# Optimization experiments

Hardware: AMD Instinct MI355X
Metric: run time of the kernel (lower is better)

## Reference

```python
import jax, jax.numpy as jnp
import numpy as np

HIDDEN = 1024
HEADS = 16
HEAD_DIM = HIDDEN // HEADS


def setup_inputs() -> dict:
    key = jax.random.key(0)
    ks = jax.random.split(key, 9)
    B, S = 2, 2048
    std = 1.0 / np.sqrt(HIDDEN)
    inp = {
        'hidden_states': jax.random.normal(ks[0], (B, S, HIDDEN), dtype=jnp.float32),
        'attention_mask': jnp.ones((B, S), dtype=jnp.int32),
        'wq': jax.random.normal(ks[1], (HIDDEN, HIDDEN), dtype=jnp.float32) * std,
        'bq': jnp.zeros((HIDDEN,), dtype=jnp.float32),
        'wk': jax.random.normal(ks[2], (HIDDEN, HIDDEN), dtype=jnp.float32) * std,
        'bk': jnp.zeros((HIDDEN,), dtype=jnp.float32),
        'wv': jax.random.normal(ks[3], (HIDDEN, HIDDEN), dtype=jnp.float32) * std,
        'bv': jnp.zeros((HIDDEN,), dtype=jnp.float32),
        'wo': jax.random.normal(ks[4], (HIDDEN, HIDDEN), dtype=jnp.float32) * std,
        'bo': jnp.zeros((HIDDEN,), dtype=jnp.float32),
    }
    return inp


def reference(hidden_states, attention_mask, wq, bq, wk, bk, wv, bv, wo, bo):
    B, S, H = hidden_states.shape
    def heads(x):  # [B,S,H] -> [B,nh,S,hd]
        return x.reshape(B, S, HEADS, HEAD_DIM).transpose(0, 2, 1, 3)
    q = heads(hidden_states @ wq + bq)
    k = heads(hidden_states @ wk + bk)
    v = heads(hidden_states @ wv + bv)
    scores = jnp.einsum('bhqd,bhkd->bhqk', q, k) / np.sqrt(HEAD_DIM).astype(np.float32)
    causal = jnp.tril(jnp.ones((S, S), dtype=bool))  # True = keep
    keep = causal[None, None] & (attention_mask[:, None, None, :] != 0)
    scores = jnp.where(keep, scores, -jnp.inf)
    probs = jax.nn.softmax(scores, axis=-1)
    out = jnp.einsum('bhqk,bhkd->bhqd', probs, v)  # [B,nh,S,hd]
    out = out.transpose(0, 2, 1, 3).reshape(B, S, H)
    return out @ wo + bo
```

## Files before the change

kernel.cpp:

```cpp
#include <hip/hip_runtime.h>

#define HID   1024
#define SLEN  2048
#define NHEAD 16
#define HDIM  64
#define SC2L  0.18033688f

typedef unsigned short u16;
typedef _Float16 f16;
using bf16x8 = __attribute__((ext_vector_type(8))) short;
using f16x4  = __attribute__((ext_vector_type(4))) f16;
using f16x8  = __attribute__((ext_vector_type(8))) f16;
using f32x4  = __attribute__((ext_vector_type(4))) float;

typedef __attribute__((address_space(1))) void gvoid;
typedef __attribute__((address_space(3))) void lvoid;

__device__ __forceinline__ u16 f2bf(float f) {
  union { float f; unsigned u; } v; v.f = f;
  unsigned u = v.u;
  return (u16)((u + 0x7fffu + ((u >> 16) & 1u)) >> 16);
}
__device__ __forceinline__ float bf2f(u16 b) {
  union { unsigned u; float f; } v; v.u = ((unsigned)b) << 16;
  return v.f;
}

__device__ __forceinline__ void async_ld16(const u16* g, u16* l) {
  __builtin_amdgcn_global_load_lds((gvoid*)g, (lvoid*)l, 16, 0, 0);
}

__global__ __launch_bounds__(256) void prep_kernel(const float* __restrict__ x,
                                                   const float* __restrict__ wq,
                                                   const float* __restrict__ wk,
                                                   const float* __restrict__ wv,
                                                   const float* __restrict__ wo,
                                                   u16* __restrict__ xb,
                                                   u16* __restrict__ wt) {
  const int tid = threadIdx.x;
  if (blockIdx.z == 4) {
    const int bid = blockIdx.y * 32 + blockIdx.x;
#pragma unroll
    for (int it = 0; it < 4; ++it) {
      const int i = bid * 1024 + it * 256 + tid;
      float4 v = ((const float4*)x)[i];
      ushort4 o;
      o.x = f2bf(v.x); o.y = f2bf(v.y); o.z = f2bf(v.z); o.w = f2bf(v.w);
      ((ushort4*)xb)[i] = o;
    }
    return;
  }
  const float* src = (blockIdx.z == 0) ? wq : (blockIdx.z == 1) ? wk
                   : (blockIdx.z == 2) ? wv : wo;
  u16* dst = wt + (size_t)blockIdx.z * (HID * HID);
  __shared__ float tile[32][33];
  const int n0 = blockIdx.x * 32, k0 = blockIdx.y * 32;
  const int xx = tid & 31, yy = tid >> 5;
  for (int i = yy; i < 32; i += 8)
    tile[i][xx] = src[(size_t)(k0 + i) * HID + n0 + xx];
  __syncthreads();
  for (int i = yy; i < 32; i += 8)
    dst[(size_t)(n0 + i) * HID + k0 + xx] = f2bf(tile[xx][i]);
}

__global__ __launch_bounds__(256) void gemm_qkv_kernel(const u16* __restrict__ A,
                                                       const u16* __restrict__ Bt,
                                                       const float* __restrict__ bq,
                                                       const float* __restrict__ bk,
                                                       const float* __restrict__ bv,
                                                       u16* __restrict__ Qb,
                                                       u16* __restrict__ Kb,
                                                       u16* __restrict__ Vb) {
  __shared__ u16 sA[128 * 32];
  __shared__ u16 sB[128 * 32];
  const int tid  = threadIdx.x;
  const int wave = tid >> 6, lane = tid & 63;
  const int quad = lane >> 4, l16 = lane & 15;
  const int n0g = blockIdx.x * 128;
  const int region = blockIdx.x >> 3;
  const int colbase = (blockIdx.x & 7) * 128;
  const int m0 = blockIdx.y * 128;
  const int wm = (wave & 1) * 64, wn = (wave >> 1) * 64;

  f32x4 acc[4][4] = {};
  const int srow = lane >> 2;
  const int scol = (lane & 3) * 8;

  for (int kt = 0; kt < HID; kt += 32) {
    __syncthreads();
    for (int c = wave; c < 8; c += 4) {
      async_ld16(A  + (size_t)(m0  + c * 16 + srow) * HID + kt + scol, &sA[c * 512]);
      async_ld16(Bt + (size_t)(n0g + c * 16 + srow) * HID + kt + scol, &sB[c * 512]);
    }
    __syncthreads();

    bf16x8 af[4], bfr[4];
#pragma unroll
    for (int t = 0; t < 4; ++t) {
      af[t]  = *(const bf16x8*)&sA[(wm + t * 16 + l16) * 32 + quad * 8];
      bfr[t] = *(const bf16x8*)&sB[(wn + t * 16 + l16) * 32 + quad * 8];
    }
#pragma unroll
    for (int mt = 0; mt < 4; ++mt)
#pragma unroll
      for (int nt = 0; nt < 4; ++nt)
        acc[mt][nt] = __builtin_amdgcn_mfma_f32_16x16x32_bf16(af[mt], bfr[nt],
                                                              acc[mt][nt], 0, 0, 0);
  }

  const float* bias = (region == 0) ? bq : (region == 1) ? bk : bv;
  u16* C = (region == 0) ? Qb : (region == 1) ? Kb : Vb;
  float bvv[4];
#pragma unroll
  for (int nt = 0; nt < 4; ++nt) bvv[nt] = bias[colbase + wn + nt * 16 + l16];
#pragma unroll
  for (int mt = 0; mt < 4; ++mt)
#pragma unroll
    for (int r = 0; r < 4; ++r) {
      const int row = m0 + wm + mt * 16 + quad * 4 + r;
#pragma unroll
      for (int nt = 0; nt < 4; ++nt) {
        const int col = colbase + wn + nt * 16 + l16;
        C[(size_t)row * HID + col] = f2bf(acc[mt][nt][r] + bvv[nt]);
      }
    }
}

__global__ __launch_bounds__(256) void gemm_o_kernel(const u16* __restrict__ A,
                                                     const u16* __restrict__ Bt,
                                                     const float* __restrict__ bias,
                                                     float* __restrict__ Cf) {
  __shared__ u16 sA[64 * 32];
  __shared__ u16 sB[128 * 32];
  const int tid  = threadIdx.x;
  const int wave = tid >> 6, lane = tid & 63;
  const int quad = lane >> 4, l16 = lane & 15;
  const int n0 = blockIdx.x * 128;
  const int m0 = blockIdx.y * 64;
  const int wn = wave * 32;

  f32x4 acc[4][2] = {};
  const int srow = lane >> 2;
  const int scol = (lane & 3) * 8;

  for (int kt = 0; kt < HID; kt += 32) {
    __syncthreads();
    for (int c = wave; c < 12; c += 4) {
      if (c < 4) async_ld16(A  + (size_t)(m0 + c * 16 + srow) * HID + kt + scol, &sA[c * 512]);
      else       async_ld16(Bt + (size_t)(n0 + (c - 4) * 16 + srow) * HID + kt + scol,
                            &sB[(c - 4) * 512]);
    }
    __syncthreads();

    bf16x8 af[4], bfr[2];
#pragma unroll
    for (int t = 0; t < 4; ++t)
      af[t] = *(const bf16x8*)&sA[(t * 16 + l16) * 32 + quad * 8];
#pragma unroll
    for (int t = 0; t < 2; ++t)
      bfr[t] = *(const bf16x8*)&sB[(wn + t * 16 + l16) * 32 + quad * 8];
#pragma unroll
    for (int mt = 0; mt < 4; ++mt)
#pragma unroll
      for (int nt = 0; nt < 2; ++nt)
        acc[mt][nt] = __builtin_amdgcn_mfma_f32_16x16x32_bf16(af[mt], bfr[nt],
                                                              acc[mt][nt], 0, 0, 0);
  }

  float bvv[2];
#pragma unroll
  for (int nt = 0; nt < 2; ++nt) bvv[nt] = bias[n0 + wn + nt * 16 + l16];
#pragma unroll
  for (int mt = 0; mt < 4; ++mt)
#pragma unroll
    for (int r = 0; r < 4; ++r) {
      const int row = m0 + mt * 16 + quad * 4 + r;
#pragma unroll
      for (int nt = 0; nt < 2; ++nt)
        Cf[(size_t)row * HID + n0 + wn + nt * 16 + l16] = acc[mt][nt][r] + bvv[nt];
    }
}

__global__ __launch_bounds__(256) void transpose_v_kernel(const u16* __restrict__ V,
                                                          u16* __restrict__ Vt) {
  const int s0 = blockIdx.x * 64, h = blockIdx.y, b = blockIdx.z;
  __shared__ u16 sh[64 * 72];
  const int tid = threadIdx.x;
#pragma unroll
  for (int i = 0; i < 2; ++i) {
    const int id = tid + i * 256;
    const int row = id >> 3, c = id & 7;
    *(bf16x8*)&sh[row * 72 + c * 8] =
        *(const bf16x8*)(V + (size_t)(b * SLEN + s0 + row) * HID + h * HDIM + c * 8);
  }
  __syncthreads();
#pragma unroll
  for (int i = 0; i < 2; ++i) {
    const int id = tid + i * 256;
    const int d = id >> 3, c = id & 7;
    ushort4 out2[2];
    u16* op = (u16*)out2;
#pragma unroll
    for (int e = 0; e < 8; ++e) {
      const int p = c * 8 + e;
      const int nt = (p >> 2) & 3, qd = p >> 4, jj = p & 3;
      const int s_local = nt * 16 + qd * 4 + jj;
      f16 hv = (f16)bf2f(sh[s_local * 72 + d]);
      union { f16 h; u16 u; } cv; cv.h = hv;
      op[e] = cv.u;
    }
    *(bf16x8*)(Vt + (size_t)((b * NHEAD + h) * HDIM + d) * SLEN + s0 + c * 8) =
        *(bf16x8*)out2;
  }
}

__global__ __launch_bounds__(256, 4) void flash_attn_kernel(const u16* __restrict__ Q,
                                                            const u16* __restrict__ K,
                                                            const u16* __restrict__ Vt,
                                                            const int* __restrict__ mask,
                                                            u16* __restrict__ O) {
  const int h = blockIdx.y, b = blockIdx.z;
  const int qt = (blockIdx.x + 2 * h + b) & 31;
  const int tid  = threadIdx.x;
  const int wave = tid >> 6, lane = tid & 63;
  const int quad = lane >> 4, l16 = lane & 15;
  const int mrow = wave * 16;
  const int q0 = qt * 64;

  __shared__ u16 Ks[2][64 * 72];
  __shared__ u16 Vts[2][64 * 72];
  __shared__ float maskadd[2][64];

  const int prow = tid >> 3;
  const int pcol = (tid & 7) * 8;

  const u16* Kh  = K  + (size_t)b * SLEN * HID + h * HDIM;
  const u16* Vth = Vt + (size_t)((b * NHEAD + h) * HDIM) * SLEN;

  const u16* qbase = Q + (size_t)(b * SLEN + q0 + mrow + l16) * HID + h * HDIM + quad * 8;
  const bf16x8 qa0 = *(const bf16x8*)qbase;
  const bf16x8 qa1 = *(const bf16x8*)(qbase + 32);

  f32x4 oacc[4] = {};
  float l_run = 0.f;

  bf16x8 kr0, kr1, vr0, vr1;
  int mreg = 0;
  {
    kr0 = *(const bf16x8*)(Kh + (size_t)prow * HID + pcol);
    kr1 = *(const bf16x8*)(Kh + (size_t)(prow + 32) * HID + pcol);
    vr0 = *(const bf16x8*)(Vth + (size_t)prow * SLEN + pcol);
    vr1 = *(const bf16x8*)(Vth + (size_t)(prow + 32) * SLEN + pcol);
    if (tid < 64) mreg = mask[b * SLEN + tid];
  }

  for (int j = 0; j <= qt; ++j) {
    const int buf = j & 1;
    *(bf16x8*)&Ks[buf][prow * 72 + pcol]         = kr0;
    *(bf16x8*)&Ks[buf][(prow + 32) * 72 + pcol]  = kr1;
    *(bf16x8*)&Vts[buf][prow * 72 + pcol]        = vr0;
    *(bf16x8*)&Vts[buf][(prow + 32) * 72 + pcol] = vr1;
    if (tid < 64) maskadd[buf][tid] = mreg ? 0.f : -1e30f;
    __syncthreads();

    if (j < qt) {
      kr0 = *(const bf16x8*)(Kh + (size_t)((j + 1) * 64 + prow) * HID + pcol);
      kr1 = *(const bf16x8*)(Kh + (size_t)((j + 1) * 64 + prow + 32) * HID + pcol);
      vr0 = *(const bf16x8*)(Vth + (size_t)prow * SLEN + (j + 1) * 64 + pcol);
      vr1 = *(const bf16x8*)(Vth + (size_t)(prow + 32) * SLEN + (j + 1) * 64 + pcol);
      if (tid < 64) mreg = mask[b * SLEN + (j + 1) * 64 + tid];
    }

    float p[4][4];
#pragma unroll
    for (int nt = 0; nt < 4; ++nt) {
      const bf16x8 kb0 = *(const bf16x8*)&Ks[buf][(nt * 16 + l16) * 72 + quad * 8];
      const bf16x8 kb1 = *(const bf16x8*)&Ks[buf][(nt * 16 + l16) * 72 + 32 + quad * 8];
      f32x4 z = {0.f, 0.f, 0.f, 0.f};
      z = __builtin_amdgcn_mfma_f32_16x16x32_bf16(kb0, qa0, z, 0, 0, 0);
      z = __builtin_amdgcn_mfma_f32_16x16x32_bf16(kb1, qa1, z, 0, 0, 0);
      const float4 ma = *(const float4*)&maskadd[buf][nt * 16 + quad * 4];
      const float* map = (const float*)&ma;
#pragma unroll
      for (int r = 0; r < 4; ++r)
        p[nt][r] = exp2f(fmaf(z[r], SC2L, map[r]));
    }
    if (j == qt) {
      const int qloc = mrow + l16;
#pragma unroll
      for (int nt = 0; nt < 4; ++nt)
#pragma unroll
        for (int r = 0; r < 4; ++r)
          if (nt * 16 + quad * 4 + r > qloc) p[nt][r] = 0.f;
    }

    f16x4 pb[4];
#pragma unroll
    for (int nt = 0; nt < 4; ++nt) {
      l_run += (p[nt][0] + p[nt][1]) + (p[nt][2] + p[nt][3]);
      pb[nt][0] = (f16)p[nt][0]; pb[nt][1] = (f16)p[nt][1];
      pb[nt][2] = (f16)p[nt][2]; pb[nt][3] = (f16)p[nt][3];
    }

#pragma unroll
    for (int mt = 0; mt < 4; ++mt) {
      const int vbase = (mt * 16 + l16) * 72 + quad * 16;
      const f16x8 v01 = *(const f16x8*)&Vts[buf][vbase];
      const f16x8 v23 = *(const f16x8*)&Vts[buf][vbase + 8];
      const f16x4 a0 = __builtin_shufflevector(v01, v01, 0, 1, 2, 3);
      const f16x4 a1 = __builtin_shufflevector(v01, v01, 4, 5, 6, 7);
      const f16x4 a2 = __builtin_shufflevector(v23, v23, 0, 1, 2, 3);
      const f16x4 a3 = __builtin_shufflevector(v23, v23, 4, 5, 6, 7);
      oacc[mt] = __builtin_amdgcn_mfma_f32_16x16x16f16(a0, pb[0], oacc[mt], 0, 0, 0);
      oacc[mt] = __builtin_amdgcn_mfma_f32_16x16x16f16(a1, pb[1], oacc[mt], 0, 0, 0);
      oacc[mt] = __builtin_amdgcn_mfma_f32_16x16x16f16(a2, pb[2], oacc[mt], 0, 0, 0);
      oacc[mt] = __builtin_amdgcn_mfma_f32_16x16x16f16(a3, pb[3], oacc[mt], 0, 0, 0);
    }
  }

  l_run += __shfl_xor(l_run, 16);
  l_run += __shfl_xor(l_run, 32);
  const float inv = 1.f / l_run;

  const int q = q0 + mrow + l16;
#pragma unroll
  for (int mt = 0; mt < 4; ++mt) {
    ushort4 o;
    o.x = f2bf(oacc[mt][0] * inv);
    o.y = f2bf(oacc[mt][1] * inv);
    o.z = f2bf(oacc[mt][2] * inv);
    o.w = f2bf(oacc[mt][3] * inv);
    *(ushort4*)(O + (size_t)(b * SLEN + q) * HID + h * HDIM + mt * 16 + quad * 4) = o;
  }
}

extern "C" void kernel_launch(void* const* d_in, const int* in_sizes, int n_in,
                              void* d_out, int out_size, void* d_ws, size_t ws_size,
                              hipStream_t stream) {
  const float* x    = (const float*)d_in[0];
  const int*   mask = (const int*)d_in[1];
  const float* wq   = (const float*)d_in[2];
  const float* bq   = (const float*)d_in[3];
  const float* wk   = (const float*)d_in[4];
  const float* bk   = (const float*)d_in[5];
  const float* wv   = (const float*)d_in[6];
  const float* bv   = (const float*)d_in[7];
  const float* wo   = (const float*)d_in[8];
  const float* bo   = (const float*)d_in[9];
  float* out = (float*)d_out;

  char* ws = (char*)d_ws;
  u16* XBF = (u16*)(ws);
  u16* WT  = (u16*)(ws + (8u  << 20));
  u16* QBF = (u16*)(ws + (16u << 20));
  u16* KBF = (u16*)(ws + (24u << 20));
  u16* VBF = (u16*)(ws + (32u << 20));
  u16* VTT = (u16*)(ws);
  u16* ATT = (u16*)(ws + (32u << 20));

  prep_kernel<<<dim3(32, 32, 5), 256, 0, stream>>>(x, wq, wk, wv, wo, XBF, WT);
  gemm_qkv_kernel<<<dim3(24, 32), 256, 0, stream>>>(XBF, WT, bq, bk, bv, QBF, KBF, VBF);
  transpose_v_kernel<<<dim3(32, NHEAD, 2), 256, 0, stream>>>(VBF, VTT);
  flash_attn_kernel<<<dim3(32, NHEAD, 2), 256, 0, stream>>>(QBF, KBF, VTT, mask, ATT);
  gemm_o_kernel<<<dim3(8, 64), 256, 0, stream>>>(ATT, WT + (3u << 20), bo, out);
}
```

Measured before the change: 216.2 us.

## Fuse V transpose into attention, split KV across waves, pair causal q-tiles

The separate V-transpose kernel is removed. The attention kernel now transposes V and converts it to fp16 inside shared memory while staging each tile. Each block handles two query tiles (qt and 31-qt) to balance causal work, and halves the grid. Within a tile, each wave takes a 16-key slice of the KV block for all 64 queries instead of 16 queries over all keys, so partial outputs and row sums must be combined through shared memory at the end. In exchange it carries more accumulator registers (occupancy hint lowered to 2), scattered 2-byte LDS stores, and an extra reduction with several barriers.

```diff
diff --git a/kernel.cpp b/kernel.cpp
--- a/kernel.cpp
+++ b/kernel.cpp
@@ -5,12 +5,13 @@
 #define NHEAD 16
 #define HDIM  64
 #define SC2L  0.18033688f
+#define KPAD  72
+#define VPAD  68
 
 typedef unsigned short u16;
 typedef _Float16 f16;
 using bf16x8 = __attribute__((ext_vector_type(8))) short;
 using f16x4  = __attribute__((ext_vector_type(4))) f16;
-using f16x8  = __attribute__((ext_vector_type(8))) f16;
 using f32x4  = __attribute__((ext_vector_type(4))) float;
 
 typedef __attribute__((address_space(1))) void gvoid;
@@ -21,9 +22,10 @@
   unsigned u = v.u;
   return (u16)((u + 0x7fffu + ((u >> 16) & 1u)) >> 16);
 }
-__device__ __forceinline__ float bf2f(u16 b) {
+__device__ __forceinline__ u16 bf2h(u16 b) {
   union { unsigned u; float f; } v; v.u = ((unsigned)b) << 16;
-  return v.f;
+  union { f16 h; u16 u; } c; c.h = (f16)v.f;
+  return c.u;
 }
 
 __device__ __forceinline__ void async_ld16(const u16* g, u16* l) {
@@ -181,156 +183,168 @@
     }
 }
 
-__global__ __launch_bounds__(256) void transpose_v_kernel(const u16* __restrict__ V,
-                                                          u16* __restrict__ Vt) {
-  const int s0 = blockIdx.x * 64, h = blockIdx.y, b = blockIdx.z;
-  __shared__ u16 sh[64 * 72];
-  const int tid = threadIdx.x;
-#pragma unroll
-  for (int i = 0; i < 2; ++i) {
-    const int id = tid + i * 256;
-    const int row = id >> 3, c = id & 7;
-    *(bf16x8*)&sh[row * 72 + c * 8] =
-        *(const bf16x8*)(V + (size_t)(b * SLEN + s0 + row) * HID + h * HDIM + c * 8);
-  }
-  __syncthreads();
-#pragma unroll
-  for (int i = 0; i < 2; ++i) {
-    const int id = tid + i * 256;
-    const int d = id >> 3, c = id & 7;
-    ushort4 out2[2];
-    u16* op = (u16*)out2;
-#pragma unroll
-    for (int e = 0; e < 8; ++e) {
-      const int p = c * 8 + e;
-      const int nt = (p >> 2) & 3, qd = p >> 4, jj = p & 3;
-      const int s_local = nt * 16 + qd * 4 + jj;
-      f16 hv = (f16)bf2f(sh[s_local * 72 + d]);
-      union { f16 h; u16 u; } cv; cv.h = hv;
-      op[e] = cv.u;
-    }
-    *(bf16x8*)(Vt + (size_t)((b * NHEAD + h) * HDIM + d) * SLEN + s0 + c * 8) =
-        *(bf16x8*)out2;
-  }
-}
-
-__global__ __launch_bounds__(256, 4) void flash_attn_kernel(const u16* __restrict__ Q,
+__global__ __launch_bounds__(256, 2) void flash_attn_kernel(const u16* __restrict__ Q,
                                                             const u16* __restrict__ K,
-                                                            const u16* __restrict__ Vt,
+                                                            const u16* __restrict__ V,
                                                             const int* __restrict__ mask,
                                                             u16* __restrict__ O) {
-  const int h = blockIdx.y, b = blockIdx.z;
-  const int qt = (blockIdx.x + 2 * h + b) & 31;
+  const int xb = blockIdx.x, h = blockIdx.y, b = blockIdx.z;
   const int tid  = threadIdx.x;
   const int wave = tid >> 6, lane = tid & 63;
   const int quad = lane >> 4, l16 = lane & 15;
-  const int mrow = wave * 16;
-  const int q0 = qt * 64;
-
-  __shared__ u16 Ks[2][64 * 72];
-  __shared__ u16 Vts[2][64 * 72];
+
+  __shared__ u16 Ks[2][64 * KPAD];
+  __shared__ u16 Vt[2][64 * VPAD];
   __shared__ float maskadd[2][64];
-
-  const int prow = tid >> 3;
-  const int pcol = (tid & 7) * 8;
-
-  const u16* Kh  = K  + (size_t)b * SLEN * HID + h * HDIM;
-  const u16* Vth = Vt + (size_t)((b * NHEAD + h) * HDIM) * SLEN;
-
-  const u16* qbase = Q + (size_t)(b * SLEN + q0 + mrow + l16) * HID + h * HDIM + quad * 8;
-  const bf16x8 qa0 = *(const bf16x8*)qbase;
-  const bf16x8 qa1 = *(const bf16x8*)(qbase + 32);
-
-  f32x4 oacc[4] = {};
-  float l_run = 0.f;
-
-  bf16x8 kr0, kr1, vr0, vr1;
-  int mreg = 0;
-  {
-    kr0 = *(const bf16x8*)(Kh + (size_t)prow * HID + pcol);
-    kr1 = *(const bf16x8*)(Kh + (size_t)(prow + 32) * HID + pcol);
-    vr0 = *(const bf16x8*)(Vth + (size_t)prow * SLEN + pcol);
-    vr1 = *(const bf16x8*)(Vth + (size_t)(prow + 32) * SLEN + pcol);
-    if (tid < 64) mreg = mask[b * SLEN + tid];
-  }
-
-  for (int j = 0; j <= qt; ++j) {
-    const int buf = j & 1;
-    *(bf16x8*)&Ks[buf][prow * 72 + pcol]         = kr0;
-    *(bf16x8*)&Ks[buf][(prow + 32) * 72 + pcol]  = kr1;
-    *(bf16x8*)&Vts[buf][prow * 72 + pcol]        = vr0;
-    *(bf16x8*)&Vts[buf][(prow + 32) * 72 + pcol] = vr1;
-    if (tid < 64) maskadd[buf][tid] = mreg ? 0.f : -1e30f;
-    __syncthreads();
-
-    if (j < qt) {
-      kr0 = *(const bf16x8*)(Kh + (size_t)((j + 1) * 64 + prow) * HID + pcol);
-      kr1 = *(const bf16x8*)(Kh + (size_t)((j + 1) * 64 + prow + 32) * HID + pcol);
-      vr0 = *(const bf16x8*)(Vth + (size_t)prow * SLEN + (j + 1) * 64 + pcol);
-      vr1 = *(const bf16x8*)(Vth + (size_t)(prow + 32) * SLEN + (j + 1) * 64 + pcol);
-      if (tid < 64) mreg = mask[b * SLEN + (j + 1) * 64 + tid];
-    }
-
-    float p[4][4];
+  __shared__ float lbuf[4][64];
+  float* Obuf0 = (float*)&Ks[0][0];
+  float* Obuf1 = (float*)&Vt[0][0];
+
+  const u16* Kh = K + (size_t)b * SLEN * HID + h * HDIM;
+  const u16* Vh = V + (size_t)b * SLEN * HID + h * HDIM;
+
+  const int srow = tid >> 2;
+  const int sc8  = (tid & 3) * 8;
+
+  for (int phase = 0; phase < 2; ++phase) {
+    const int qt = phase ? (31 - xb) : xb;
+    const int q0 = qt * 64;
+
+    bf16x8 qb[4][2];
 #pragma unroll
     for (int nt = 0; nt < 4; ++nt) {
-      const bf16x8 kb0 = *(const bf16x8*)&Ks[buf][(nt * 16 + l16) * 72 + quad * 8];
-      const bf16x8 kb1 = *(const bf16x8*)&Ks[buf][(nt * 16 + l16) * 72 + 32 + quad * 8];
-      f32x4 z = {0.f, 0.f, 0.f, 0.f};
-      z = __builtin_amdgcn_mfma_f32_16x16x32_bf16(kb0, qa0, z, 0, 0, 0);
-      z = __builtin_amdgcn_mfma_f32_16x16x32_bf16(kb1, qa1, z, 0, 0, 0);
-      const float4 ma = *(const float4*)&maskadd[buf][nt * 16 + quad * 4];
+      const u16* qp = Q + (size_t)(b * SLEN + q0 + nt * 16 + l16) * HID + h * HDIM + quad * 8;
+      qb[nt][0] = *(const bf16x8*)qp;
+      qb[nt][1] = *(const bf16x8*)(qp + 32);
+    }
+
+    f32x4 oacc[4][4] = {};
+    float l_part[4] = {0.f, 0.f, 0.f, 0.f};
+
+    bf16x8 kr0, kr1, vr0, vr1;
+    int mreg = 0;
+    {
+      const u16* kg = Kh + (size_t)srow * HID + sc8;
+      kr0 = *(const bf16x8*)kg;  kr1 = *(const bf16x8*)(kg + 32);
+      const u16* vg = Vh + (size_t)srow * HID + sc8;
+      vr0 = *(const bf16x8*)vg;  vr1 = *(const bf16x8*)(vg + 32);
+      if (tid < 64) mreg = mask[b * SLEN + tid];
+    }
+
+    for (int j = 0; j <= qt; ++j) {
+      const int buf = j & 1;
+      *(bf16x8*)&Ks[buf][srow * KPAD + sc8]      = kr0;
+      *(bf16x8*)&Ks[buf][srow * KPAD + sc8 + 32] = kr1;
+      {
+        const u16* v0 = (const u16*)&vr0;
+        const u16* v1 = (const u16*)&vr1;
+#pragma unroll
+        for (int e = 0; e < 8; ++e) {
+          Vt[buf][(sc8 + e) * VPAD + srow]      = bf2h(v0[e]);
+          Vt[buf][(sc8 + e + 32) * VPAD + srow] = bf2h(v1[e]);
+        }
+      }
+      if (tid < 64) maskadd[buf][tid] = mreg ? 0.f : -1e30f;
+      __syncthreads();
+
+      if (j < qt) {
+        const u16* kg = Kh + (size_t)((j + 1) * 64 + srow) * HID + sc8;
+        kr0 = *(const bf16x8*)kg;  kr1 = *(const bf16x8*)(kg + 32);
+        const u16* vg = Vh + (size_t)((j + 1) * 64 + srow) * HID + sc8;
+        vr0 = *(const bf16x8*)vg;  vr1 = *(const bf16x8*)(vg + 32);
+        if (tid < 64) mreg = mask[b * SLEN + (j + 1) * 64 + tid];
+      }
+
+      const bf16x8 ka0 = *(const bf16x8*)&Ks[buf][(wave * 16 + l16) * KPAD + quad * 8];
+      const bf16x8 ka1 = *(const bf16x8*)&Ks[buf][(wave * 16 + l16) * KPAD + quad * 8 + 32];
+      const float4 ma  = *(const float4*)&maskadd[buf][wave * 16 + quad * 4];
       const float* map = (const float*)&ma;
-#pragma unroll
-      for (int r = 0; r < 4; ++r)
-        p[nt][r] = exp2f(fmaf(z[r], SC2L, map[r]));
-    }
-    if (j == qt) {
-      const int qloc = mrow + l16;
-#pragma unroll
-      for (int nt = 0; nt < 4; ++nt)
+
+      float p[4][4];
+#pragma unroll
+      for (int nt = 0; nt < 4; ++nt) {
+        f32x4 z = {0.f, 0.f, 0.f, 0.f};
+        z = __builtin_amdgcn_mfma_f32_16x16x32_bf16(ka0, qb[nt][0], z, 0, 0, 0);
+        z = __builtin_amdgcn_mfma_f32_16x16x32_bf16(ka1, qb[nt][1], z, 0, 0, 0);
 #pragma unroll
         for (int r = 0; r < 4; ++r)
-          if (nt * 16 + quad * 4 + r > qloc) p[nt][r] = 0.f;
-    }
-
-    f16x4 pb[4];
+          p[nt][r] = exp2f(fmaf(z[r], SC2L, map[r]));
+      }
+      if (j == qt) {
+#pragma unroll
+        for (int nt = 0; nt < 4; ++nt)
+#pragma unroll
+          for (int r = 0; r < 4; ++r)
+            if (wave * 16 + quad * 4 + r > nt * 16 + l16) p[nt][r] = 0.f;
+      }
+
+      f16x4 pb[4];
+#pragma unroll
+      for (int nt = 0; nt < 4; ++nt) {
+        l_part[nt] += (p[nt][0] + p[nt][1]) + (p[nt][2] + p[nt][3]);
+        pb[nt][0] = (f16)p[nt][0]; pb[nt][1] = (f16)p[nt][1];
+        pb[nt][2] = (f16)p[nt][2]; pb[nt][3] = (f16)p[nt][3];
+      }
+
+#pragma unroll
+      for (int dt = 0; dt < 4; ++dt) {
+        const f16x4 va = *(const f16x4*)&Vt[buf][(dt * 16 + l16) * VPAD + wave * 16 + quad * 4];
+#pragma unroll
+        for (int nt = 0; nt < 4; ++nt)
+          oacc[dt][nt] = __builtin_amdgcn_mfma_f32_16x16x16f16(va, pb[nt], oacc[dt][nt], 0, 0, 0);
+      }
+    }
+
 #pragma unroll
     for (int nt = 0; nt < 4; ++nt) {
-      l_run += (p[nt][0] + p[nt][1]) + (p[nt][2] + p[nt][3]);
-      pb[nt][0] = (f16)p[nt][0]; pb[nt][1] = (f16)p[nt][1];
-      pb[nt][2] = (f16)p[nt][2]; pb[nt][3] = (f16)p[nt][3];
-    }
-
-#pragma unroll
-    for (int mt = 0; mt < 4; ++mt) {
-      const int vbase = (mt * 16 + l16) * 72 + quad * 16;
-      const f16x8 v01 = *(const f16x8*)&Vts[buf][vbase];
-      const f16x8 v23 = *(const f16x8*)&Vts[buf][vbase + 8];
-      const f16x4 a0 = __builtin_shufflevector(v01, v01, 0, 1, 2, 3);
-      const f16x4 a1 = __builtin_shufflevector(v01, v01, 4, 5, 6, 7);
-      const f16x4 a2 = __builtin_shufflevector(v23, v23, 0, 1, 2, 3);
-      const f16x4 a3 = __builtin_shufflevector(v23, v23, 4, 5, 6, 7);
-      oacc[mt] = __builtin_amdgcn_mfma_f32_16x16x16f16(a0, pb[0], oacc[mt], 0, 0, 0);
-      oacc[mt] = __builtin_amdgcn_mfma_f32_16x16x16f16(a1, pb[1], oacc[mt], 0, 0, 0);
-      oacc[mt] = __builtin_amdgcn_mfma_f32_16x16x16f16(a2, pb[2], oacc[mt], 0, 0, 0);
-      oacc[mt] = __builtin_amdgcn_mfma_f32_16x16x16f16(a3, pb[3], oacc[mt], 0, 0, 0);
-    }
-  }
-
-  l_run += __shfl_xor(l_run, 16);
-  l_run += __shfl_xor(l_run, 32);
-  const float inv = 1.f / l_run;
-
-  const int q = q0 + mrow + l16;
-#pragma unroll
-  for (int mt = 0; mt < 4; ++mt) {
-    ushort4 o;
-    o.x = f2bf(oacc[mt][0] * inv);
-    o.y = f2bf(oacc[mt][1] * inv);
-    o.z = f2bf(oacc[mt][2] * inv);
-    o.w = f2bf(oacc[mt][3] * inv);
-    *(ushort4*)(O + (size_t)(b * SLEN + q) * HID + h * HDIM + mt * 16 + quad * 4) = o;
+      l_part[nt] += __shfl_xor(l_part[nt], 16);
+      l_part[nt] += __shfl_xor(l_part[nt], 32);
+    }
+    __syncthreads();
+
+    if (quad == 0)
+#pragma unroll
+      for (int nt = 0; nt < 4; ++nt) lbuf[wave][nt * 16 + l16] = l_part[nt];
+
+    if ((wave & 1) == 0) {
+      float* ob = (wave == 0) ? Obuf0 : Obuf1;
+#pragma unroll
+      for (int dt = 0; dt < 4; ++dt)
+#pragma unroll
+        for (int nt = 0; nt < 4; ++nt)
+#pragma unroll
+          for (int r = 0; r < 4; ++r)
+            ob[(dt * 16 + quad * 4 + r) * 65 + nt * 16 + l16] = oacc[dt][nt][r];
+    }
+    __syncthreads();
+    if (wave & 1) {
+      float* ob = (wave == 1) ? Obuf0 : Obuf1;
+#pragma unroll
+      for (int dt = 0; dt < 4; ++dt)
+#pragma unroll
+        for (int nt = 0; nt < 4; ++nt)
+#pragma unroll
+          for (int r = 0; r < 4; ++r)
+            ob[(dt * 16 + quad * 4 + r) * 65 + nt * 16 + l16] += oacc[dt][nt][r];
+    }
+    __syncthreads();
+
+    {
+      const int q  = tid >> 2;
+      const int dc = tid & 3;
+      const float l = lbuf[0][q] + lbuf[1][q] + lbuf[2][q] + lbuf[3][q];
+      const float inv = 1.f / l;
+      u16 ob[16];
+#pragma unroll
+      for (int e = 0; e < 16; ++e) {
+        const int d = dc * 16 + e;
+        ob[e] = f2bf((Obuf0[d * 65 + q] + Obuf1[d * 65 + q]) * inv);
+      }
+      u16* op = O + (size_t)(b * SLEN + q0 + q) * HID + h * HDIM + dc * 16;
+      *(bf16x8*)op       = *(bf16x8*)&ob[0];
+      *(bf16x8*)(op + 8) = *(bf16x8*)&ob[8];
+    }
+    __syncthreads();
   }
 }
 
@@ -355,12 +369,10 @@
   u16* QBF = (u16*)(ws + (16u << 20));
   u16* KBF = (u16*)(ws + (24u << 20));
   u16* VBF = (u16*)(ws + (32u << 20));
-  u16* VTT = (u16*)(ws);
-  u16* ATT = (u16*)(ws + (32u << 20));
+  u16* ATT = (u16*)(ws);
 
   prep_kernel<<<dim3(32, 32, 5), 256, 0, stream>>>(x, wq, wk, wv, wo, XBF, WT);
   gemm_qkv_kernel<<<dim3(24, 32), 256, 0, stream>>>(XBF, WT, bq, bk, bv, QBF, KBF, VBF);
-  transpose_v_kernel<<<dim3(32, NHEAD, 2), 256, 0, stream>>>(VBF, VTT);
-  flash_attn_kernel<<<dim3(32, NHEAD, 2), 256, 0, stream>>>(QBF, KBF, VTT, mask, ATT);
+  flash_attn_kernel<<<dim3(16, NHEAD, 2), 256, 0, stream>>>(QBF, KBF, VBF, mask, ATT);
   gemm_o_kernel<<<dim3(8, 64), 256, 0, stream>>>(ATT, WT + (3u << 20), bo, out);
 }
```

New measurement: 207.8 us. 3.9% less time.
